# Kernel optimization log

Hardware: AMD Instinct MI355X
Metric: run time of the kernel (lower is better)

The kernel has to match this reference:

```python
import jax, jax.numpy as jnp
import numpy as np

MODEL_DIM = 1024
HEAD_DIM = 64
NUM_HEADS = 16
FF_DIM = 4 * MODEL_DIM
ROT_DIM = 32  # max(head_dim // 2, 32)
FUSED = (NUM_HEADS * HEAD_DIM,) * 3 + (FF_DIM,) * 2
B, S = 2, 2048


def rotate_half(x):
    x1, x2 = jnp.split(x, 2, axis=-1)
    return jnp.concatenate([-x2, x1], axis=-1)


def rope_freqs(seq_len, dim=ROT_DIM, max_period=10000.0):
    inv_freq = 1.0 / max_period ** (jnp.arange(0, dim, 2, dtype=jnp.float32) / dim)
    freqs = jnp.arange(seq_len, dtype=jnp.float32)[:, None] * inv_freq[None, :]
    return jnp.concatenate([freqs, freqs], axis=-1)  # [S, dim]


def setup_inputs() -> dict:
    key = jax.random.key(0)
    ks = jax.random.split(key, 10)
    d = MODEL_DIM
    s_in = (sum(FUSED) ** -0.5)
    return {
        "inputs": jax.random.normal(ks[0], (B, S, d), jnp.float32),
        "time_embeds": jax.random.normal(ks[1], (B, 1, d), jnp.float32),
        "ln_w": jnp.ones((d,), jnp.float32),
        "ln_b": jnp.zeros((d,), jnp.float32),
        "cond_w": jax.random.normal(ks[2], (d, 2 * d), jnp.float32) * (d ** -0.5),
        "cond_b": jnp.zeros((2 * d,), jnp.float32),
        "w_in": jax.random.normal(ks[3], (d, sum(FUSED)), jnp.float32) * (d ** -0.5),
        "w_attn": jax.random.normal(ks[4], (NUM_HEADS * HEAD_DIM, d), jnp.float32) * ((NUM_HEADS * HEAD_DIM) ** -0.5),
        "w_ff": jax.random.normal(ks[5], (FF_DIM, d), jnp.float32) * (FF_DIM ** -0.5),
        "b_ff": jnp.zeros((d,), jnp.float32),
    }


def reference(inputs, time_embeds, ln_w, ln_b, cond_w, cond_b, w_in, w_attn, w_ff, b_ff):
    # LayerNorm
    mu = jnp.mean(inputs, axis=-1, keepdims=True)
    var = jnp.mean(jnp.square(inputs - mu), axis=-1, keepdims=True)
    units = (inputs - mu) * jax.lax.rsqrt(var + 1e-5) * ln_w + ln_b

    # FiLM conditioning
    cond = jax.nn.silu(time_embeds) @ cond_w + cond_b  # [B,1,2D]
    scale, bias = jnp.split(cond, 2, axis=-1)
    units = (1.0 + scale) * units + bias

    # Fused projection -> q, k, v, ff, ff_gate
    proj = units @ w_in
    splits = np.cumsum(FUSED)[:-1].tolist()
    q, k, v, ff, ff_gate = jnp.split(proj, splits, axis=-1)

    def split_heads(x):  # [B,S,H*hd] -> [B,H,S,hd]
        return x.reshape(B, S, NUM_HEADS, HEAD_DIM).transpose(0, 2, 1, 3)

    q, k, v = split_heads(q), split_heads(k), split_heads(v)

    # Rotary on first ROT_DIM dims of q, k
    freqs = rope_freqs(S)  # [S, ROT_DIM]
    cos, sin = jnp.cos(freqs), jnp.sin(freqs)

    def rope(x):
        xl, xr = x[..., :ROT_DIM], x[..., ROT_DIM:]
        xl = xl * cos + rotate_half(xl) * sin
        return jnp.concatenate([xl, xr], axis=-1)

    q, k = rope(q), rope(k)

    # Attention (full score matrix, manual softmax, as original)
    score = jnp.einsum("bhsd,bhSd->bhsS", q, k) * (HEAD_DIM ** -0.5)
    weight = jax.nn.softmax(score, axis=-1)
    attn = jnp.einsum("bhsS,bhSd->bhsd", weight, v)
    concat = attn.transpose(0, 2, 1, 3).reshape(B, S, NUM_HEADS * HEAD_DIM)
    attn_out = concat @ w_attn

    # GeGLU FF
    ff_out = (ff * jax.nn.gelu(ff_gate, approximate=True)) @ w_ff + b_ff

    return inputs + attn_out + ff_out
```

## Files before the change

kernel.cpp:

```cpp
#include <hip/hip_runtime.h>
#include <hip/hip_bf16.h>

typedef __attribute__((ext_vector_type(8))) __bf16 bf16x8;
typedef __attribute__((ext_vector_type(4))) float f32x4;
typedef unsigned short u16;
typedef unsigned int u32;

#define DMODEL 1024
#define SLEN   2048
#define NPROJ  11264
#define NFUSE  5120
#define MROWS  4096

__device__ __forceinline__ float b2f(u16 u){ u32 v=((u32)u)<<16; float f; __builtin_memcpy(&f,&v,4); return f; }
__device__ __forceinline__ u16 f2b(float f){ u32 u; __builtin_memcpy(&u,&f,4); u32 r=u+0x7fffu+((u>>16)&1u); return (u16)(r>>16); }
__device__ __forceinline__ float fexp2(float x){ return __builtin_amdgcn_exp2f(x); }

__device__ __forceinline__ void gload16(const void* g, void* l){
  __builtin_amdgcn_global_load_lds((__attribute__((address_space(1))) u32*)g,
                                   (__attribute__((address_space(3))) u32*)l, 16, 0, 0);
}

__global__ __launch_bounds__(256) void k_transpose_all(const float* __restrict__ w_in,
                                                       const float* __restrict__ w_attn,
                                                       const float* __restrict__ w_ff,
                                                       u16* __restrict__ w_inT,
                                                       u16* __restrict__ w_fusedT){
  __shared__ float tile[32][33];
  int bid = blockIdx.x;
  const float* src; u16* dst; int N, ldd, coloff, nx, remap, tix;
  if (bid < 11264){ tix=bid;       nx=352; src=w_in;   N=NPROJ;  dst=w_inT;    ldd=DMODEL; coloff=0;    remap=1; }
  else if (bid < 12288){ tix=bid-11264; nx=32; src=w_attn; N=DMODEL; dst=w_fusedT; ldd=NFUSE; coloff=0;    remap=0; }
  else {            tix=bid-12288; nx=32;  src=w_ff;   N=DMODEL; dst=w_fusedT; ldd=NFUSE;  coloff=1024; remap=0; }
  int n0 = (tix%nx)*32, k0 = (tix/nx)*32;
  int tx = threadIdx.x & 31, ty = threadIdx.x >> 5;
  int srccol;
  if (remap && (n0 + tx) >= 3072){
    int c = n0 + tx - 3072;
    int q = c >> 5, o = c & 31;
    srccol = (o < 16) ? (3072 + 16*q + o) : (7168 + 16*q + (o-16));
  } else srccol = n0 + tx;
  #pragma unroll
  for (int r=0;r<4;r++)
    tile[ty*4+r][tx] = src[(size_t)(k0+ty*4+r)*N + srccol];
  __syncthreads();
  #pragma unroll
  for (int r=0;r<4;r++){
    int n = ty*4+r;
    dst[(size_t)(n0+n)*ldd + coloff + k0 + tx] = f2b(tile[tx][n]);
  }
}

__global__ __launch_bounds__(256) void k_rope_table(float* __restrict__ tab){
  int idx = blockIdx.x*256 + threadIdx.x;
  if (idx >= SLEN*16) return;
  int s = idx >> 4, i = idx & 15;
  float inv = powf(10000.f, -(float)i/16.f);
  float f = (float)s * inv;
  tab[s*32 + i]      = cosf(f);
  tab[s*32 + 16 + i] = sinf(f);
}

__global__ __launch_bounds__(256) void k_cond(const float* __restrict__ te, const float* __restrict__ cw,
                                              const float* __restrict__ cb, float* __restrict__ cond){
  __shared__ float sl[DMODEL];
  int b = blockIdx.y, t = threadIdx.x;
  for (int i=t;i<DMODEL;i+=256){ float x = te[b*DMODEL+i]; sl[i] = x/(1.f+expf(-x)); }
  __syncthreads();
  int n = blockIdx.x*256 + t;
  float acc = 0.f;
  for (int k=0;k<DMODEL;k++) acc += sl[k]*cw[(size_t)k*2048 + n];
  cond[b*2048+n] = acc + cb[n];
}

__global__ __launch_bounds__(256) void k_ln(const float* __restrict__ x, const float* __restrict__ lw,
                                            const float* __restrict__ lb, const float* __restrict__ cond,
                                            u16* __restrict__ units){
  int row = blockIdx.x; int b = row >> 11;
  int t = threadIdx.x;
  const float4 v = *(const float4*)(x + (size_t)row*DMODEL + t*4);
  float s = v.x+v.y+v.z+v.w;
  float q = v.x*v.x+v.y*v.y+v.z*v.z+v.w*v.w;
  #pragma unroll
  for (int off=32; off; off>>=1){ s += __shfl_xor(s,off); q += __shfl_xor(q,off); }
  __shared__ float red[8];
  int w = t>>6, l = t&63;
  if (l==0){ red[w]=s; red[4+w]=q; }
  __syncthreads();
  float S = red[0]+red[1]+red[2]+red[3];
  float Q = red[4]+red[5]+red[6]+red[7];
  float mu = S*(1.f/1024.f);
  float var = Q*(1.f/1024.f) - mu*mu;
  float rstd = rsqrtf(var + 1e-5f);
  int c0 = t*4;
  u16 o[4];
  const float* vf = (const float*)&v;
  #pragma unroll
  for (int i=0;i<4;i++){
    int c = c0+i;
    float nrm = (vf[i]-mu)*rstd*lw[c] + lb[c];
    float outv = (1.f + cond[b*2048 + c])*nrm + cond[b*2048 + 1024 + c];
    o[i] = f2b(outv);
  }
  u32 p0 = (u32)o[0] | ((u32)o[1]<<16);
  u32 p1 = (u32)o[2] | ((u32)o[3]<<16);
  uint2 pk; pk.x = p0; pk.y = p1;
  *(uint2*)(units + (size_t)row*DMODEL + c0) = pk;
}

template<int BM,int BN,int WM,int WN,int NBUF,int MINW,int EPI>
__global__ __launch_bounds__(WM*WN*64, MINW) void k_gemm_pipe(
    const u16* __restrict__ A, const u16* __restrict__ Bt, int K, int lda, int ldb,
    const float* __restrict__ tab, u16* __restrict__ qh, u16* __restrict__ kh,
    u16* __restrict__ vq, u16* __restrict__ afinal, u16* __restrict__ pb)
{
  constexpr int THREADS = WM*WN*64;
  constexpr int MR = BM/WM/16, NR = BN/WN/16;
  constexpr int BUFE = (BM+BN)*32;
  __shared__ __attribute__((aligned(16))) u16 lds[NBUF*BUFE];
  int t = threadIdx.x, w = t>>6, l = t&63;
  int wr = w/WN, wc = w%WN;
  int lane16 = l&15, lg = l>>4;

  int nbx = gridDim.x, nby = gridDim.y;
  int wg = blockIdx.y*nbx + blockIdx.x;
  int nwg = nbx*nby;
  int cpx = nwg>>3;
  int swz = (wg&7)*cpx + (wg>>3);
  int bx, by;
  if constexpr (EPI==0){ bx = swz / nby; by = swz - bx*nby; }
  else                { bx = swz % nbx; by = swz / nbx; }

  size_t m0 = (size_t)by*BM, n0 = (size_t)bx*BN;
  int koff = (EPI==1) ? blockIdx.z*2560 : 0;
  const u16* Ag = A + m0*lda + koff;
  const u16* Bg = Bt + n0*ldb + koff;

  f32x4 zero = {0.f,0.f,0.f,0.f};
  f32x4 acc[MR][NR];
  #pragma unroll
  for (int i=0;i<MR;i++)
    #pragma unroll
    for (int j=0;j<NR;j++) acc[i][j] = zero;

  const int ntiles = K/32;

  auto STAGE = [&](int tt, int buf){
    int k0 = tt*32;
    char* Ad = (char*)lds + (size_t)buf*(BUFE*2);
    char* Bd = Ad + BM*64;
    #pragma unroll
    for (int i=0;i<2;i++){
      int s = i*THREADS + t;
      int r = s>>2, g = s&3;
      int src = (g ^ ((r>>1)&3))*8;
      gload16(Ag + (size_t)r*lda + k0 + src, Ad + (i*THREADS + w*64)*16);
      gload16(Bg + (size_t)r*ldb + k0 + src, Bd + (i*THREADS + w*64)*16);
    }
  };

  #pragma unroll
  for (int p=0;p<NBUF-1;p++) STAGE(p, p);

  int cur = 0;
  for (int kt=0; kt<ntiles; ++kt){
    int rem = ntiles-1-kt;
    if (rem>=1)      asm volatile("s_waitcnt vmcnt(4)" ::: "memory");
    else             asm volatile("s_waitcnt vmcnt(0)" ::: "memory");
    __builtin_amdgcn_s_barrier();
    const u16* As = lds + (size_t)cur*BUFE;
    const u16* Bs = As + BM*32;
    bf16x8 af[MR], bf[NR];
    #pragma unroll
    for (int i=0;i<MR;i++){
      int r = wr*(MR*16) + i*16 + lane16;
      int g = lg ^ ((r>>1)&3);
      af[i] = *(const bf16x8*)(As + r*32 + g*8);
    }
    #pragma unroll
    for (int j=0;j<NR;j++){
      int r = wc*(NR*16) + j*16 + lane16;
      int g = lg ^ ((r>>1)&3);
      bf[j] = *(const bf16x8*)(Bs + r*32 + g*8);
    }
    int st = kt + NBUF-1;
    if (st < ntiles) STAGE(st, (cur==0)?(NBUF-1):(cur-1));
    __builtin_amdgcn_s_setprio(1);
    #pragma unroll
    for (int i=0;i<MR;i++)
      #pragma unroll
      for (int j=0;j<NR;j++)
        acc[i][j] = __builtin_amdgcn_mfma_f32_16x16x32_bf16(af[i], bf[j], acc[i][j], 0,0,0);
    __builtin_amdgcn_s_setprio(0);
    __builtin_amdgcn_sched_barrier(0);
    cur = (cur+1==NBUF)?0:(cur+1);
  }

  if constexpr (EPI==0){
    int region = (n0 < 3072) ? (int)(n0>>10) : 3;
    if (region<=1){
      u16* dst = (region==0)? qh : kh;
      float sc = (region==0)? 0.125f*1.44269504f : 1.0f;
      int h = (int)((n0 & 1023)>>6) + wc;
      int d = lane16;
      #pragma unroll
      for (int i=0;i<MR;i++){
        #pragma unroll
        for (int r=0;r<4;r++){
          int row = (int)m0 + wr*(MR*16) + i*16 + lg*4 + r;
          int bb = row>>11, s = row&2047;
          float cs = tab[s*32+d], sn = tab[s*32+16+d];
          float x0 = acc[i][0][r], x1 = acc[i][1][r];
          size_t base = ((size_t)(bb*16+h)*SLEN + s)*64;
          dst[base+d]    = f2b((x0*cs - x1*sn)*sc);
          dst[base+16+d] = f2b((x1*cs + x0*sn)*sc);
          dst[base+32+d] = f2b(acc[i][2][r]*sc);
          dst[base+48+d] = f2b(acc[i][3][r]*sc);
        }
      }
    } else if (region==2){
      #pragma unroll
      for (int i=0;i<MR;i++)
        #pragma unroll
        for (int j=0;j<NR;j++){
          int cv = (int)(n0-2048) + wc*(NR*16) + j*16 + lane16;
          #pragma unroll
          for (int r=0;r<4;r++){
            int row = (int)m0 + wr*(MR*16) + i*16 + lg*4 + r;
            vq[(size_t)row*DMODEL + cv] = f2b(acc[i][j][r]);
          }
        }
    } else {
      int fbase = (int)((n0-3072)>>1) + wc*(NR*8) + lane16;
      #pragma unroll
      for (int i=0;i<MR;i++)
        #pragma unroll
        for (int p=0;p<NR/2;p++){
          int col = 1024 + fbase + p*16;
          #pragma unroll
          for (int r=0;r<4;r++){
            int row = (int)m0 + wr*(MR*16) + i*16 + lg*4 + r;
            float fv = acc[i][2*p][r];
            float gv = acc[i][2*p+1][r];
            float tz = 0.7978845608f*(gv + 0.044715f*gv*gv*gv);
            float th = 1.f - 2.f/(__expf(2.f*tz)+1.f);
            afinal[(size_t)row*NFUSE + col] = f2b(fv * 0.5f*gv*(1.f+th));
          }
        }
    }
  } else {
    u16* pbs = pb + (size_t)blockIdx.z*MROWS*DMODEL;
    #pragma unroll
    for (int i=0;i<MR;i++)
      #pragma unroll
      for (int j=0;j<NR;j++){
        int col = (int)n0 + wc*(NR*16) + j*16 + lane16;
        #pragma unroll
        for (int r=0;r<4;r++){
          int row = (int)m0 + wr*(MR*16) + i*16 + lg*4 + r;
          pbs[(size_t)row*DMODEL + col] = f2b(acc[i][j][r]);
        }
      }
  }
}

__global__ __launch_bounds__(256) void k_reduce(const u16* __restrict__ pb, const float* __restrict__ resid,
                                                const float* __restrict__ bias, float* __restrict__ out){
  size_t i8 = ((size_t)blockIdx.x*256 + threadIdx.x)*8;
  uint4 a0 = *(const uint4*)(pb + i8);
  uint4 a1 = *(const uint4*)(pb + (size_t)MROWS*DMODEL + i8);
  const u16* p0 = (const u16*)&a0;
  const u16* p1 = (const u16*)&a1;
  float4 r0 = *(const float4*)(resid + i8);
  float4 r1 = *(const float4*)(resid + i8 + 4);
  int bcol = (int)(i8 & 1023);
  float4 b0 = *(const float4*)(bias + bcol);
  float4 b1 = *(const float4*)(bias + bcol + 4);
  float4 o0, o1;
  const float* rr0 = (const float*)&r0; const float* bb0 = (const float*)&b0;
  const float* rr1 = (const float*)&r1; const float* bb1 = (const float*)&b1;
  float* oo0 = (float*)&o0; float* oo1 = (float*)&o1;
  #pragma unroll
  for (int k=0;k<4;k++){
    oo0[k] = b2f(p0[k]) + b2f(p1[k]) + rr0[k] + bb0[k];
    oo1[k] = b2f(p0[4+k]) + b2f(p1[4+k]) + rr1[k] + bb1[k];
  }
  *(float4*)(out + i8)     = o0;
  *(float4*)(out + i8 + 4) = o1;
}

__global__ __launch_bounds__(256) void k_vtrans(const u16* __restrict__ vq, u16* __restrict__ vt){
  int b = blockIdx.z, h = blockIdx.y, s0 = blockIdx.x*64;
  int t = threadIdx.x;
  __shared__ u16 vt_lds[64][72];
  int sl = t>>2, quad = t&3;
  const u16* prow = vq + (size_t)(b*SLEN + s0 + sl)*DMODEL + h*64;
  #pragma unroll
  for (int i=0;i<16;i++){
    int d = quad*16+i;
    vt_lds[d][sl] = prow[d];
  }
  __syncthreads();
  int d = t>>2, sg = t&3;
  size_t base = ((size_t)(b*16+h)*64 + d)*SLEN + s0 + sg*16;
  #pragma unroll
  for (int i=0;i<16;i++)
    vt[base + i] = vt_lds[d][sg*16+i];
}

#define M0SHIFT 20.0f
__global__ __launch_bounds__(256,3) void k_attn(const u16* __restrict__ qh, const u16* __restrict__ kh,
                                                const u16* __restrict__ vt, u16* __restrict__ afinal){
  __shared__ __attribute__((aligned(16))) u16 Klds[2][64*64];
  __shared__ __attribute__((aligned(16))) u16 Vlds[2][64*64];
  __shared__ __attribute__((aligned(16))) u16 Plds[4][32*72];
  int p = (blockIdx.z*16 + blockIdx.y)*16 + blockIdx.x;
  int c = p&7, k = p>>3;
  int hb = c + 8*(k&3);
  int qx = k>>2;
  int b = hb>>4, h = hb&15, q0 = qx*128;
  int t = threadIdx.x, w = t>>6, l = t&63;
  int lane16 = l&15, lg = l>>4;
  size_t hoff = (size_t)hb*SLEN*64;
  const u16* Qb = qh + hoff + (size_t)(q0 + w*32)*64;
  const u16* Kb = kh + hoff;
  const u16* Vb = vt + hoff;
  bf16x8 qf[2][2];
  #pragma unroll
  for (int mi=0;mi<2;mi++)
    #pragma unroll
    for (int ks=0;ks<2;ks++)
      qf[mi][ks] = *(const bf16x8*)(Qb + (size_t)(mi*16+lane16)*64 + ks*32 + lg*8);
  bf16x8 ones;
  #pragma unroll
  for (int i=0;i<8;i++) ones[i] = (__bf16)1.0f;
  f32x4 zero = {0.f,0.f,0.f,0.f};
  f32x4 acc[2][4];
  f32x4 lacc[2];
  #pragma unroll
  for (int mi=0;mi<2;mi++){
    lacc[mi] = zero;
    #pragma unroll
    for (int n=0;n<4;n++) acc[mi][n] = zero;
  }

  auto STAGE = [&](int buf, int kv0){
    #pragma unroll
    for (int r=0;r<2;r++){
      int cc = r*256 + t;
      int row = cc>>3;
      int g = (cc&7) ^ (row&7);
      gload16(Kb + (size_t)(kv0+row)*64 + g*8, (char*)Klds[buf] + r*4096 + w*1024);
      gload16(Vb + (size_t)row*SLEN + kv0 + g*8, (char*)Vlds[buf] + r*4096 + w*1024);
    }
  };

  STAGE(0, 0);
  __syncthreads();

  for (int tile=0; tile<32; ++tile){
    int cur = tile & 1;
    if (tile+1 < 32) STAGE(cur^1, (tile+1)*64);
    f32x4 sf[2][4];
    #pragma unroll
    for (int mi=0;mi<2;mi++)
      #pragma unroll
      for (int n=0;n<4;n++) sf[mi][n] = zero;
    __builtin_amdgcn_s_setprio(1);
    #pragma unroll
    for (int n=0;n<4;n++){
      #pragma unroll
      for (int ks=0;ks<2;ks++){
        int rk = n*16 + lane16;
        int g = (ks*4 + lg) ^ (rk&7);
        bf16x8 kf = *(const bf16x8*)(Klds[cur] + rk*64 + g*8);
        sf[0][n] = __builtin_amdgcn_mfma_f32_16x16x32_bf16(qf[0][ks], kf, sf[0][n], 0,0,0);
        sf[1][n] = __builtin_amdgcn_mfma_f32_16x16x32_bf16(qf[1][ks], kf, sf[1][n], 0,0,0);
      }
    }
    __builtin_amdgcn_s_setprio(0);
    #pragma unroll
    for (int mi=0;mi<2;mi++)
      #pragma unroll
      for (int jr=0;jr<4;jr++)
        #pragma unroll
        for (int n=0;n<4;n++){
          float pv = fexp2(sf[mi][n][jr] - M0SHIFT);
          u32 u; __builtin_memcpy(&u,&pv,4);
          Plds[w][(mi*16 + lg*4 + jr)*72 + n*16 + lane16] = (u16)(u>>16);
        }
    __builtin_amdgcn_s_setprio(1);
    #pragma unroll
    for (int ks=0;ks<2;ks++){
      bf16x8 vf[4];
      #pragma unroll
      for (int n=0;n<4;n++){
        int rv = n*16 + lane16;
        int g = (ks*4 + lg) ^ (rv&7);
        vf[n] = *(const bf16x8*)(Vlds[cur] + rv*64 + g*8);
      }
      #pragma unroll
      for (int mi=0;mi<2;mi++){
        bf16x8 pa = *(const bf16x8*)(&Plds[w][(mi*16 + lane16)*72 + ks*32 + lg*8]);
        #pragma unroll
        for (int n=0;n<4;n++)
          acc[mi][n] = __builtin_amdgcn_mfma_f32_16x16x32_bf16(pa, vf[n], acc[mi][n], 0,0,0);
        lacc[mi] = __builtin_amdgcn_mfma_f32_16x16x32_bf16(pa, ones, lacc[mi], 0,0,0);
      }
    }
    __builtin_amdgcn_s_setprio(0);
    __syncthreads();
  }
  #pragma unroll
  for (int mi=0;mi<2;mi++){
    float inv[4];
    #pragma unroll
    for (int jr=0;jr<4;jr++) inv[jr] = 1.f/lacc[mi][jr];
    #pragma unroll
    for (int n=0;n<4;n++)
      #pragma unroll
      for (int jr=0;jr<4;jr++){
        int srow = q0 + w*32 + mi*16 + lg*4 + jr;
        int col = h*64 + n*16 + lane16;
        afinal[(size_t)(b*SLEN+srow)*NFUSE + col] = f2b(acc[mi][n][jr]*inv[jr]);
      }
  }
}

extern "C" void kernel_launch(void* const* d_in, const int* in_sizes, int n_in,
                              void* d_out, int out_size, void* d_ws, size_t ws_size,
                              hipStream_t stream) {
  const float* inputs = (const float*)d_in[0];
  const float* te     = (const float*)d_in[1];
  const float* ln_w   = (const float*)d_in[2];
  const float* ln_b   = (const float*)d_in[3];
  const float* cond_w = (const float*)d_in[4];
  const float* cond_b = (const float*)d_in[5];
  const float* w_in   = (const float*)d_in[6];
  const float* w_attn = (const float*)d_in[7];
  const float* w_ff   = (const float*)d_in[8];
  const float* b_ff   = (const float*)d_in[9];
  float* out = (float*)d_out;

  char* ws = (char*)d_ws;
  size_t off = 0;
  auto alloc = [&](size_t n)->char*{ char* p = ws + off; off += (n + 255) & ~(size_t)255; return p; };
  u16*  w_inT    = (u16*)alloc((size_t)NPROJ*DMODEL*2);
  u16*  w_fusedT = (u16*)alloc((size_t)DMODEL*NFUSE*2);
  u16*  units    = (u16*)alloc((size_t)MROWS*DMODEL*2);
  u16*  qh       = (u16*)alloc((size_t)MROWS*DMODEL*2);
  u16*  kh       = (u16*)alloc((size_t)MROWS*DMODEL*2);
  u16*  vq       = (u16*)alloc((size_t)MROWS*DMODEL*2);
  u16*  vT       = (u16*)alloc((size_t)MROWS*DMODEL*2);
  u16*  afinal   = (u16*)alloc((size_t)MROWS*NFUSE*2);
  u16*  pb       = (u16*)alloc((size_t)2*MROWS*DMODEL*2);
  float* cond    = (float*)alloc(2*2048*4);
  float* ropetab = (float*)alloc((size_t)SLEN*32*4);
  (void)ws_size; (void)in_sizes; (void)n_in; (void)out_size;

  k_transpose_all<<<dim3(16384), 256, 0, stream>>>(w_in, w_attn, w_ff, w_inT, w_fusedT);
  k_rope_table<<<128, 256, 0, stream>>>(ropetab);
  k_cond<<<dim3(8,2), 256, 0, stream>>>(te, cond_w, cond_b, cond);
  k_ln<<<MROWS, 256, 0, stream>>>(inputs, ln_w, ln_b, cond, units);
  k_gemm_pipe<256,256,2,4,3,2,0><<<dim3(NPROJ/256, MROWS/256), 512, 0, stream>>>(
      units, w_inT, DMODEL, DMODEL, DMODEL, ropetab, qh, kh, vq, afinal, nullptr);
  k_vtrans<<<dim3(SLEN/64, 16, 2), 256, 0, stream>>>(vq, vT);
  k_attn<<<dim3(16, 16, 2), 256, 0, stream>>>(qh, kh, vT, afinal);
  k_gemm_pipe<128,128,2,2,3,3,1><<<dim3(DMODEL/128, MROWS/128, 2), 256, 0, stream>>>(
      afinal, w_fusedT, 2560, NFUSE, NFUSE, nullptr, nullptr, nullptr, nullptr, nullptr, pb);
  k_reduce<<<dim3(MROWS*DMODEL/2048), 256, 0, stream>>>(pb, inputs, b_ff, out);
}
```

Before: 287.0 us.

## Fuse V transpose into projection GEMM epilogue and merge prep kernels

The projection GEMM epilogue now writes V directly in the transposed [b,h,d,s] layout using packed 4-element stores, which removes the separate k_vtrans kernel and the intermediate vq buffer round trip. The rope table and FiLM cond computations are folded into the weight transpose kernel as extra blocks, cutting two launches. In exchange, the transposed stores are strided by SLEN and only 8 bytes wide, so they may coalesce less well than the old row-major writes.

```diff
diff --git a/kernel.cpp b/kernel.cpp
--- a/kernel.cpp
+++ b/kernel.cpp
@@ -21,13 +21,40 @@
                                    (__attribute__((address_space(3))) u32*)l, 16, 0, 0);
 }
 
-__global__ __launch_bounds__(256) void k_transpose_all(const float* __restrict__ w_in,
-                                                       const float* __restrict__ w_attn,
-                                                       const float* __restrict__ w_ff,
-                                                       u16* __restrict__ w_inT,
-                                                       u16* __restrict__ w_fusedT){
+__global__ __launch_bounds__(256) void k_prep(const float* __restrict__ w_in,
+                                              const float* __restrict__ w_attn,
+                                              const float* __restrict__ w_ff,
+                                              const float* __restrict__ te,
+                                              const float* __restrict__ cond_w,
+                                              const float* __restrict__ cond_b,
+                                              u16* __restrict__ w_inT,
+                                              u16* __restrict__ w_fusedT,
+                                              float* __restrict__ ropetab,
+                                              float* __restrict__ cond){
   __shared__ float tile[32][33];
+  __shared__ float sl[DMODEL];
   int bid = blockIdx.x;
+  if (bid >= 16384){
+    int xb = bid - 16384;
+    if (xb < 128){
+      int idx = xb*256 + threadIdx.x;
+      int s = idx >> 4, i = idx & 15;
+      float inv = powf(10000.f, -(float)i/16.f);
+      float f = (float)s * inv;
+      ropetab[s*32 + i]      = cosf(f);
+      ropetab[s*32 + 16 + i] = sinf(f);
+    } else {
+      int cb2 = xb - 128;
+      int b = cb2>>3, t = threadIdx.x;
+      for (int i=t;i<DMODEL;i+=256){ float x = te[b*DMODEL+i]; sl[i] = x/(1.f+expf(-x)); }
+      __syncthreads();
+      int n = (cb2&7)*256 + t;
+      float acc = 0.f;
+      for (int k=0;k<DMODEL;k++) acc += sl[k]*cond_w[(size_t)k*2048 + n];
+      cond[b*2048+n] = acc + cond_b[n];
+    }
+    return;
+  }
   const float* src; u16* dst; int N, ldd, coloff, nx, remap, tix;
   if (bid < 11264){ tix=bid;       nx=352; src=w_in;   N=NPROJ;  dst=w_inT;    ldd=DMODEL; coloff=0;    remap=1; }
   else if (bid < 12288){ tix=bid-11264; nx=32; src=w_attn; N=DMODEL; dst=w_fusedT; ldd=NFUSE; coloff=0;    remap=0; }
@@ -49,28 +76,6 @@
     int n = ty*4+r;
     dst[(size_t)(n0+n)*ldd + coloff + k0 + tx] = f2b(tile[tx][n]);
   }
-}
-
-__global__ __launch_bounds__(256) void k_rope_table(float* __restrict__ tab){
-  int idx = blockIdx.x*256 + threadIdx.x;
-  if (idx >= SLEN*16) return;
-  int s = idx >> 4, i = idx & 15;
-  float inv = powf(10000.f, -(float)i/16.f);
-  float f = (float)s * inv;
-  tab[s*32 + i]      = cosf(f);
-  tab[s*32 + 16 + i] = sinf(f);
-}
-
-__global__ __launch_bounds__(256) void k_cond(const float* __restrict__ te, const float* __restrict__ cw,
-                                              const float* __restrict__ cb, float* __restrict__ cond){
-  __shared__ float sl[DMODEL];
-  int b = blockIdx.y, t = threadIdx.x;
-  for (int i=t;i<DMODEL;i+=256){ float x = te[b*DMODEL+i]; sl[i] = x/(1.f+expf(-x)); }
-  __syncthreads();
-  int n = blockIdx.x*256 + t;
-  float acc = 0.f;
-  for (int k=0;k<DMODEL;k++) acc += sl[k]*cw[(size_t)k*2048 + n];
-  cond[b*2048+n] = acc + cb[n];
 }
 
 __global__ __launch_bounds__(256) void k_ln(const float* __restrict__ x, const float* __restrict__ lw,
@@ -112,7 +117,7 @@
 __global__ __launch_bounds__(WM*WN*64, MINW) void k_gemm_pipe(
     const u16* __restrict__ A, const u16* __restrict__ Bt, int K, int lda, int ldb,
     const float* __restrict__ tab, u16* __restrict__ qh, u16* __restrict__ kh,
-    u16* __restrict__ vq, u16* __restrict__ afinal, u16* __restrict__ pb)
+    u16* __restrict__ vt, u16* __restrict__ afinal, u16* __restrict__ pb)
 {
   constexpr int THREADS = WM*WN*64;
   constexpr int MR = BM/WM/16, NR = BN/WN/16;
@@ -220,16 +225,19 @@
       }
     } else if (region==2){
       #pragma unroll
-      for (int i=0;i<MR;i++)
-        #pragma unroll
-        for (int j=0;j<NR;j++){
-          int cv = (int)(n0-2048) + wc*(NR*16) + j*16 + lane16;
+      for (int j=0;j<NR;j++){
+        int cv = (int)(n0-2048) + wc*(NR*16) + j*16 + lane16;
+        int hh = cv>>6, dd = cv&63;
+        #pragma unroll
+        for (int i=0;i<MR;i++){
+          int row0 = (int)m0 + wr*(MR*16) + i*16 + lg*4;
+          int bb = row0>>11, s0 = row0&2047;
+          union { u16 o[4]; uint2 v; } pk2;
           #pragma unroll
-          for (int r=0;r<4;r++){
-            int row = (int)m0 + wr*(MR*16) + i*16 + lg*4 + r;
-            vq[(size_t)row*DMODEL + cv] = f2b(acc[i][j][r]);
-          }
+          for (int r=0;r<4;r++) pk2.o[r] = f2b(acc[i][j][r]);
+          *(uint2*)(vt + ((size_t)(bb*16+hh)*64 + dd)*SLEN + s0) = pk2.v;
         }
+      }
     } else {
       int fbase = (int)((n0-3072)>>1) + wc*(NR*8) + lane16;
       #pragma unroll
@@ -287,25 +295,6 @@
   }
   *(float4*)(out + i8)     = o0;
   *(float4*)(out + i8 + 4) = o1;
-}
-
-__global__ __launch_bounds__(256) void k_vtrans(const u16* __restrict__ vq, u16* __restrict__ vt){
-  int b = blockIdx.z, h = blockIdx.y, s0 = blockIdx.x*64;
-  int t = threadIdx.x;
-  __shared__ u16 vt_lds[64][72];
-  int sl = t>>2, quad = t&3;
-  const u16* prow = vq + (size_t)(b*SLEN + s0 + sl)*DMODEL + h*64;
-  #pragma unroll
-  for (int i=0;i<16;i++){
-    int d = quad*16+i;
-    vt_lds[d][sl] = prow[d];
-  }
-  __syncthreads();
-  int d = t>>2, sg = t&3;
-  size_t base = ((size_t)(b*16+h)*64 + d)*SLEN + s0 + sg*16;
-  #pragma unroll
-  for (int i=0;i<16;i++)
-    vt[base + i] = vt_lds[d][sg*16+i];
 }
 
 #define M0SHIFT 20.0f
@@ -450,7 +439,6 @@
   u16*  units    = (u16*)alloc((size_t)MROWS*DMODEL*2);
   u16*  qh       = (u16*)alloc((size_t)MROWS*DMODEL*2);
   u16*  kh       = (u16*)alloc((size_t)MROWS*DMODEL*2);
-  u16*  vq       = (u16*)alloc((size_t)MROWS*DMODEL*2);
   u16*  vT       = (u16*)alloc((size_t)MROWS*DMODEL*2);
   u16*  afinal   = (u16*)alloc((size_t)MROWS*NFUSE*2);
   u16*  pb       = (u16*)alloc((size_t)2*MROWS*DMODEL*2);
@@ -458,13 +446,11 @@
   float* ropetab = (float*)alloc((size_t)SLEN*32*4);
   (void)ws_size; (void)in_sizes; (void)n_in; (void)out_size;
 
-  k_transpose_all<<<dim3(16384), 256, 0, stream>>>(w_in, w_attn, w_ff, w_inT, w_fusedT);
-  k_rope_table<<<128, 256, 0, stream>>>(ropetab);
-  k_cond<<<dim3(8,2), 256, 0, stream>>>(te, cond_w, cond_b, cond);
+  k_prep<<<dim3(16384+128+16), 256, 0, stream>>>(w_in, w_attn, w_ff, te, cond_w, cond_b,
+                                                 w_inT, w_fusedT, ropetab, cond);
   k_ln<<<MROWS, 256, 0, stream>>>(inputs, ln_w, ln_b, cond, units);
   k_gemm_pipe<256,256,2,4,3,2,0><<<dim3(NPROJ/256, MROWS/256), 512, 0, stream>>>(
-      units, w_inT, DMODEL, DMODEL, DMODEL, ropetab, qh, kh, vq, afinal, nullptr);
-  k_vtrans<<<dim3(SLEN/64, 16, 2), 256, 0, stream>>>(vq, vT);
+      units, w_inT, DMODEL, DMODEL, DMODEL, ropetab, qh, kh, vT, afinal, nullptr);
   k_attn<<<dim3(16, 16, 2), 256, 0, stream>>>(qh, kh, vT, afinal);
   k_gemm_pipe<128,128,2,2,3,3,1><<<dim3(DMODEL/128, MROWS/128, 2), 256, 0, stream>>>(
       afinal, w_fusedT, 2560, NFUSE, NFUSE, nullptr, nullptr, nullptr, nullptr, nullptr, pb);
```

After: 282.2 us. No clear change (-1.7%).
